# Kernel tuning notes

Measured on AMD Instinct MI355X. Metric: run time of the kernel, lower is better.

The kernel has to match this reference:

```python
import jax, jax.numpy as jnp
import numpy as np

B, D, H, W = 64, 256, 32, 32
K, DC = 1024, 128  # codebook size, codebook dim = D // 2
BETA = 0.25


def setup_inputs() -> dict:
    key = jax.random.key(0)
    ks = jax.random.split(key, 4)
    return {
        "x": jax.random.normal(ks[0], (B, D, H, W), dtype=jnp.float32),
        "pre_W": jax.random.normal(ks[1], (DC, D), dtype=jnp.float32) * (1.0 / np.sqrt(D)),
        "pre_b": jnp.zeros((DC,), dtype=jnp.float32),
        "post_W": jax.random.normal(ks[2], (D, DC), dtype=jnp.float32) * (1.0 / np.sqrt(DC)),
        "post_b": jnp.zeros((D,), dtype=jnp.float32),
        "lookup_table": jax.random.normal(ks[3], (K, DC), dtype=jnp.float32) * (1.0 / np.sqrt(DC)),
    }


def reference(x, pre_W, pre_b, post_W, post_b, lookup_table):
    sg = jax.lax.stop_gradient
    b, d, h, w = x.shape
    # pre-quant 1x1 conv: [b, d, h, w] -> [b, dc, h, w]
    z = jnp.einsum("bchw,oc->bohw", x, pre_W) + pre_b[None, :, None, None]
    # flatten tokens: [b*h*w, dc]
    zf = z.transpose(0, 2, 3, 1).reshape(-1, DC)
    # squared distances to codebook (argmin identical to cdist argmin)
    d2 = (
        jnp.sum(zf * zf, axis=1, keepdims=True)
        - 2.0 * zf @ lookup_table.T
        + jnp.sum(lookup_table * lookup_table, axis=1)[None, :]
    )  # [N, K]
    q = jnp.argmin(d2, axis=1)  # [N]
    x_e = lookup_table[q].reshape(b, h, w, DC).transpose(0, 3, 1, 2)  # [b, dc, h, w]
    # losses (enable_ema_update = False path)
    codebook_loss = jnp.mean((sg(z) - x_e) ** 2)
    commitment_loss = BETA * jnp.mean((z - sg(x_e)) ** 2)
    loss = (1.0 - BETA) * codebook_loss + commitment_loss
    # straight-through estimator
    z_st = z + sg(x_e - z)
    # post-quant 1x1 conv: [b, dc, h, w] -> [b, d, h, w]
    out = jnp.einsum("bchw,oc->bohw", z_st, post_W) + post_b[None, :, None, None]
    # perplexity from empirical code usage
    counts = jnp.zeros((K,), dtype=jnp.float32).at[q].add(1.0)
    e_mean = counts / q.shape[0]
    perplexity = jnp.exp(-jnp.sum(e_mean * jnp.log(e_mean + 1e-10)))
    q_map = q.reshape(b, h, w)
    return out, loss, q_map, perplexity
```

## Files before the change

### kernel.cpp

```cpp
#include <hip/hip_runtime.h>
#include <cstdint>

#define NB   64
#define ND   256
#define NHW  1024
#define NTOK 65536
#define NDC  128
#define NK   1024

#define OFF_LOSS 16777216
#define OFF_Q    16777217
#define OFF_PERP 16842753

#define GAPTHR 1e-3f
#define NEGINF (-3.402823466e38f)

typedef short short8 __attribute__((ext_vector_type(8)));
typedef float f32x4 __attribute__((ext_vector_type(4)));

__device__ __forceinline__ unsigned short f2bf(float f) {
  unsigned u = __float_as_uint(f);
  u += 0x7FFFu + ((u >> 16) & 1u);
  return (unsigned short)(u >> 16);
}
__device__ __forceinline__ float bf2f(unsigned short h) {
  return __uint_as_float(((unsigned)h) << 16);
}

__device__ __forceinline__ void gll16(const void* g, void* l) {
  __builtin_amdgcn_global_load_lds(
      (const __attribute__((address_space(1))) unsigned int*)g,
      (__attribute__((address_space(3))) unsigned int*)l, 16, 0, 0);
}

__global__ __launch_bounds__(256) void k_init(
    const float* __restrict__ lut, const float* __restrict__ preW,
    const float* __restrict__ postW,
    unsigned short* __restrict__ ch,
    unsigned short* __restrict__ pwh, unsigned short* __restrict__ pwl,
    unsigned short* __restrict__ qwh, unsigned short* __restrict__ qwl,
    float* __restrict__ nhn, double* __restrict__ cn2d,
    int* __restrict__ counts, double* __restrict__ lossAcc, int* __restrict__ ctr) {
  int tid = blockIdx.x * 256 + threadIdx.x;
  int stride = gridDim.x * 256;
  for (int i = tid; i < NK * NDC; i += stride) {
    int code = i >> 7, c = i & 127;
    float f = lut[i];
    unsigned short h1 = f2bf(f);
    float r = f - bf2f(h1);
    ch[code * 256 + c] = h1;
    ch[code * 256 + 128 + c] = f2bf(r);
  }
  for (int i = tid; i < NDC * ND; i += stride) {
    float f = preW[i];
    unsigned u = __float_as_uint(f);
    float lf = f - __uint_as_float(u & 0xffff0000u);
    pwh[i] = (unsigned short)(u >> 16);
    pwl[i] = (unsigned short)(__float_as_uint(lf) >> 16);
  }
  for (int i = tid; i < ND * NDC; i += stride) {
    float f = postW[i];
    unsigned u = __float_as_uint(f);
    float lf = f - __uint_as_float(u & 0xffff0000u);
    qwh[i] = (unsigned short)(u >> 16);
    qwl[i] = (unsigned short)(__float_as_uint(lf) >> 16);
  }
  if (tid < NK) {
    float s = 0.f;
    double sd = 0.0;
    for (int c = 0; c < NDC; c++) {
      float v = lut[tid * NDC + c];
      s = fmaf(v, v, s);
      sd = fma((double)v, (double)v, sd);
    }
    nhn[tid] = -0.5f * s;
    cn2d[tid] = sd;
    counts[tid] = 0;
  }
  if (tid == 0) { *lossAcc = 0.0; *ctr = 0; }
}

__global__ __launch_bounds__(256, 2) void k_preconv(
    const float* __restrict__ x, const unsigned short* __restrict__ pwh,
    const unsigned short* __restrict__ pwl, const float* __restrict__ pre_b,
    float* __restrict__ zf) {
  int bx = blockIdx.x;
  int b = bx >> 3, p0 = (bx & 7) * 128;
  int tid = threadIdx.x;
  int lane = tid & 63, w = tid >> 6;
  int g = lane >> 4, l15 = lane & 15;
  const float* xb = x + (size_t)b * (ND * NHW);
  f32x4 acc[8][2];
  #pragma unroll
  for (int rt = 0; rt < 8; ++rt)
    #pragma unroll
    for (int ct = 0; ct < 2; ++ct) acc[rt][ct] = (f32x4){0.f, 0.f, 0.f, 0.f};

  for (int ks = 0; ks < 8; ++ks) {
    int k0 = ks * 32;
    short8 bh[2], bl[2];
    #pragma unroll
    for (int ct = 0; ct < 2; ++ct) {
      int p = p0 + w * 32 + ct * 16 + l15;
      float xv[8];
      #pragma unroll
      for (int j = 0; j < 8; ++j)
        xv[j] = xb[(k0 + g * 8 + j) * NHW + p];
      #pragma unroll
      for (int j = 0; j < 8; ++j) {
        unsigned u = __float_as_uint(xv[j]);
        float lf = xv[j] - __uint_as_float(u & 0xffff0000u);
        bh[ct][j] = (short)(u >> 16);
        bl[ct][j] = (short)(__float_as_uint(lf) >> 16);
      }
    }
    #pragma unroll
    for (int rt = 0; rt < 8; ++rt) {
      short8 ah = *reinterpret_cast<const short8*>(&pwh[(rt * 16 + l15) * ND + k0 + g * 8]);
      short8 al = *reinterpret_cast<const short8*>(&pwl[(rt * 16 + l15) * ND + k0 + g * 8]);
      #pragma unroll
      for (int ct = 0; ct < 2; ++ct) {
        acc[rt][ct] = __builtin_amdgcn_mfma_f32_16x16x32_bf16(ah, bh[ct], acc[rt][ct], 0, 0, 0);
        acc[rt][ct] = __builtin_amdgcn_mfma_f32_16x16x32_bf16(ah, bl[ct], acc[rt][ct], 0, 0, 0);
        acc[rt][ct] = __builtin_amdgcn_mfma_f32_16x16x32_bf16(al, bh[ct], acc[rt][ct], 0, 0, 0);
      }
    }
  }
  #pragma unroll
  for (int rt = 0; rt < 8; ++rt) {
    float4 bb = *reinterpret_cast<const float4*>(&pre_b[rt * 16 + g * 4]);
    #pragma unroll
    for (int ct = 0; ct < 2; ++ct) {
      int n = bx * 128 + w * 32 + ct * 16 + l15;
      float4 v;
      v.x = acc[rt][ct][0] + bb.x;
      v.y = acc[rt][ct][1] + bb.y;
      v.z = acc[rt][ct][2] + bb.z;
      v.w = acc[rt][ct][3] + bb.w;
      *reinterpret_cast<float4*>(&zf[(size_t)n * NDC + rt * 16 + g * 4]) = v;
    }
  }
}

__global__ __launch_bounds__(256, 2) void k_dist(
    const float* __restrict__ zf, const unsigned short* __restrict__ ch,
    const float* __restrict__ nhn,
    int* __restrict__ q, int* __restrict__ list, int* __restrict__ ctr) {
  __shared__ __align__(16) short chbuf[2][16384];
  __shared__ float HnLds[NK];
  int tid = threadIdx.x;
  int lane = tid & 63, w = tid >> 6;
  int g = lane >> 4;
  int n0 = blockIdx.x * 128;

  for (int i = tid; i < NK; i += 256) HnLds[i] = nhn[i];

  short8 az[2][8];
  {
    int arow = lane & 15;
    #pragma unroll
    for (int rt = 0; rt < 2; ++rt) {
      const float* zr = zf + (size_t)(n0 + w * 32 + rt * 16 + arow) * NDC;
      #pragma unroll
      for (int f = 0; f < 4; ++f) {
        const float* p = zr + f * 32 + g * 8;
        float4 v0 = *reinterpret_cast<const float4*>(p);
        float4 v1 = *reinterpret_cast<const float4*>(p + 4);
        float vv[8] = {v0.x, v0.y, v0.z, v0.w, v1.x, v1.y, v1.z, v1.w};
        short8 hi, lo;
        #pragma unroll
        for (int j = 0; j < 8; ++j) {
          unsigned short h1 = f2bf(vv[j]);
          float r = vv[j] - bf2f(h1);
          hi[j] = (short)h1;
          lo[j] = (short)f2bf(r);
        }
        az[rt][f] = hi;
        az[rt][4 + f] = lo;
      }
    }
  }

  float best[2][4], sec[2][4];
  int bidx[2][4];
  #pragma unroll
  for (int rt = 0; rt < 2; ++rt)
    #pragma unroll
    for (int r = 0; r < 4; ++r) { best[rt][r] = NEGINF; sec[rt][r] = NEGINF; bidx[rt][r] = 0; }

  const char* chg = (const char*)ch;
  {
    const char* gb = chg + 0;
    #pragma unroll
    for (int rr = 0; rr < 8; ++rr) {
      int o = rr * 4096 + tid * 16;
      int so = o ^ (((o >> 9) & 7) << 4);
      gll16(gb + so, ((char*)&chbuf[0][0]) + o);
    }
  }
  asm volatile("s_waitcnt vmcnt(0)" ::: "memory");
  __syncthreads();

  int cur = 0;
  for (int chunk = 0; chunk < 16; ++chunk) {
    if (chunk < 15) {
      const char* gb = chg + (chunk + 1) * 32768;
      #pragma unroll
      for (int rr = 0; rr < 8; ++rr) {
        int o = rr * 4096 + tid * 16;
        int so = o ^ (((o >> 9) & 7) << 4);
        gll16(gb + so, ((char*)&chbuf[cur ^ 1][0]) + o);
      }
    }
    const char* cb = (const char*)&chbuf[cur][0];
    for (int ct = 0; ct < 4; ++ct) {
      int codeg = chunk * 64 + ct * 16 + (lane & 15);
      float nh = HnLds[codeg];
      short8 bc[8];
      #pragma unroll
      for (int f = 0; f < 8; ++f) {
        int byte = ((lane & 15) + ct * 16) * 512 + f * 64 + g * 16;
        byte ^= ((lane & 7) << 4);
        bc[f] = *reinterpret_cast<const short8*>(cb + byte);
      }
      f32x4 acc0 = {nh, nh, nh, nh};
      f32x4 acc1 = {nh, nh, nh, nh};
      #pragma unroll
      for (int j = 0; j < 4; ++j) {
        acc0 = __builtin_amdgcn_mfma_f32_16x16x32_bf16(az[0][j], bc[j], acc0, 0, 0, 0);
        acc1 = __builtin_amdgcn_mfma_f32_16x16x32_bf16(az[1][j], bc[j], acc1, 0, 0, 0);
        acc0 = __builtin_amdgcn_mfma_f32_16x16x32_bf16(az[0][j], bc[4 + j], acc0, 0, 0, 0);
        acc1 = __builtin_amdgcn_mfma_f32_16x16x32_bf16(az[1][j], bc[4 + j], acc1, 0, 0, 0);
        acc0 = __builtin_amdgcn_mfma_f32_16x16x32_bf16(az[0][4 + j], bc[j], acc0, 0, 0, 0);
        acc1 = __builtin_amdgcn_mfma_f32_16x16x32_bf16(az[1][4 + j], bc[j], acc1, 0, 0, 0);
      }
      #pragma unroll
      for (int r = 0; r < 4; ++r) {
        float s0 = acc0[r];
        bool t0 = s0 > best[0][r];
        bidx[0][r] = t0 ? codeg : bidx[0][r];
        sec[0][r] = fmaxf(sec[0][r], fminf(s0, best[0][r]));
        best[0][r] = fmaxf(s0, best[0][r]);
        float s1 = acc1[r];
        bool t1 = s1 > best[1][r];
        bidx[1][r] = t1 ? codeg : bidx[1][r];
        sec[1][r] = fmaxf(sec[1][r], fminf(s1, best[1][r]));
        best[1][r] = fmaxf(s1, best[1][r]);
      }
    }
    asm volatile("s_waitcnt vmcnt(0)" ::: "memory");
    __syncthreads();
    cur ^= 1;
  }

  #pragma unroll
  for (int rt = 0; rt < 2; ++rt) {
    #pragma unroll
    for (int r = 0; r < 4; ++r) {
      float b = best[rt][r];
      float s2 = sec[rt][r];
      int bi_ = bidx[rt][r];
      #pragma unroll
      for (int m = 1; m < 16; m <<= 1) {
        float ob = __shfl_xor(b, m, 64);
        float os = __shfl_xor(s2, m, 64);
        int oi = __shfl_xor(bi_, m, 64);
        float ns = fmaxf(fmaxf(s2, os), fminf(b, ob));
        bool take = (ob > b) || (ob == b && oi < bi_);
        b = take ? ob : b;
        bi_ = take ? oi : bi_;
        s2 = ns;
      }
      if ((lane & 15) == 0) {
        int token = n0 + w * 32 + rt * 16 + g * 4 + r;
        q[token] = bi_;
        if (b - s2 < GAPTHR) {
          int pos = atomicAdd(ctr, 1);
          list[pos] = token;
        }
      }
    }
  }
}

__global__ __launch_bounds__(256) void k_rescore(
    const float* __restrict__ x, const float* __restrict__ preW,
    const float* __restrict__ pre_b, const float* __restrict__ lut,
    const double* __restrict__ cn2d,
    const int* __restrict__ list, const int* __restrict__ ctr, int* __restrict__ q) {
  __shared__ float xs[4][256];
  __shared__ double zs[4][128];
  __shared__ double rd[4][256];
  __shared__ int    rc[4][256];
  int nf = *ctr;
  int tid = threadIdx.x;
  int w = tid >> 6, lane = tid & 63;
  for (int g0 = blockIdx.x * 4; g0 < nf; g0 += gridDim.x * 4) {
    int nt = nf - g0; if (nt > 4) nt = 4;
    #pragma unroll
    for (int t = 0; t < 4; ++t) {
      int token = list[g0 + (t < nt ? t : 0)];
      int b = token >> 10, p = token & 1023;
      xs[t][tid] = x[(size_t)(b * ND + tid) * NHW + p];
    }
    __syncthreads();
    #pragma unroll
    for (int rep = 0; rep < 2; ++rep) {
      int idx = rep * 256 + tid;
      int t = idx >> 7, dc = idx & 127;
      double acc = (double)pre_b[dc];
      const float* wr = preW + (size_t)dc * ND;
      #pragma unroll 4
      for (int d = 0; d < ND; d += 4) {
        float4 wv = *reinterpret_cast<const float4*>(wr + d);
        acc = fma((double)wv.x, (double)xs[t][d + 0], acc);
        acc = fma((double)wv.y, (double)xs[t][d + 1], acc);
        acc = fma((double)wv.z, (double)xs[t][d + 2], acc);
        acc = fma((double)wv.w, (double)xs[t][d + 3], acc);
      }
      zs[t][dc] = acc;
    }
    __syncthreads();
    double bd[4]; int bc_[4];
    #pragma unroll
    for (int t = 0; t < 4; ++t) { bd[t] = 1e300; bc_[t] = 0x7fffffff; }
    for (int cc = 0; cc < 4; ++cc) {
      int c = cc * 256 + tid;
      const float* cr = lut + (size_t)c * NDC;
      double a0 = 0.0, a1 = 0.0, a2 = 0.0, a3 = 0.0;
      #pragma unroll 4
      for (int k = 0; k < NDC; ++k) {
        double lc = (double)cr[k];
        a0 = fma(zs[0][k], lc, a0);
        a1 = fma(zs[1][k], lc, a1);
        a2 = fma(zs[2][k], lc, a2);
        a3 = fma(zs[3][k], lc, a3);
      }
      double cn = cn2d[c];
      double d0 = cn - 2.0 * a0; if (d0 < bd[0]) { bd[0] = d0; bc_[0] = c; }
      double d1 = cn - 2.0 * a1; if (d1 < bd[1]) { bd[1] = d1; bc_[1] = c; }
      double d2 = cn - 2.0 * a2; if (d2 < bd[2]) { bd[2] = d2; bc_[2] = c; }
      double d3 = cn - 2.0 * a3; if (d3 < bd[3]) { bd[3] = d3; bc_[3] = c; }
    }
    #pragma unroll
    for (int t = 0; t < 4; ++t) { rd[t][tid] = bd[t]; rc[t][tid] = bc_[t]; }
    __syncthreads();
    {
      double b_ = rd[w][lane]; int c_ = rc[w][lane];
      #pragma unroll
      for (int s = 64; s < 256; s += 64) {
        double ob = rd[w][lane + s]; int oc = rc[w][lane + s];
        if (ob < b_ || (ob == b_ && oc < c_)) { b_ = ob; c_ = oc; }
      }
      #pragma unroll
      for (int m = 1; m < 64; m <<= 1) {
        double ob = __shfl_xor(b_, m, 64);
        int oc = __shfl_xor(c_, m, 64);
        if (ob < b_ || (ob == b_ && oc < c_)) { b_ = ob; c_ = oc; }
      }
      if (lane == 0 && w < nt) q[list[g0 + w]] = c_;
    }
    __syncthreads();
  }
}

__global__ __launch_bounds__(256, 2) void k_post(
    const float* __restrict__ zf, const float* __restrict__ lut,
    const int* __restrict__ q, const unsigned short* __restrict__ qwh,
    const unsigned short* __restrict__ qwl, const float* __restrict__ post_b,
    float* __restrict__ out, double* __restrict__ lossAcc,
    int* __restrict__ counts, float* __restrict__ outq) {
  __shared__ float red[256];
  int bx = blockIdx.x;
  int n0 = (bx >> 1) * 128;
  int oh = (bx & 1) * 128;
  int b = n0 >> 10, p0 = n0 & 1023;
  int tid = threadIdx.x;
  int lane = tid & 63, w = tid >> 6;
  int g = lane >> 4, l15 = lane & 15;

  int qv[2];
  #pragma unroll
  for (int ct = 0; ct < 2; ++ct) qv[ct] = q[n0 + w * 32 + ct * 16 + l15];

  f32x4 acc[8][2];
  #pragma unroll
  for (int nt = 0; nt < 8; ++nt)
    #pragma unroll
    for (int ct = 0; ct < 2; ++ct) acc[nt][ct] = (f32x4){0.f, 0.f, 0.f, 0.f};

  for (int ks = 0; ks < 4; ++ks) {
    int k0 = ks * 32;
    short8 ah[2], al[2];
    #pragma unroll
    for (int ct = 0; ct < 2; ++ct) {
      const float* xr = lut + (size_t)qv[ct] * NDC + k0 + g * 8;
      float4 v0 = *reinterpret_cast<const float4*>(xr);
      float4 v1 = *reinterpret_cast<const float4*>(xr + 4);
      float vv[8] = {v0.x, v0.y, v0.z, v0.w, v1.x, v1.y, v1.z, v1.w};
      #pragma unroll
      for (int j = 0; j < 8; ++j) {
        unsigned u = __float_as_uint(vv[j]);
        float lf = vv[j] - __uint_as_float(u & 0xffff0000u);
        ah[ct][j] = (short)(u >> 16);
        al[ct][j] = (short)(__float_as_uint(lf) >> 16);
      }
    }
    #pragma unroll
    for (int nt = 0; nt < 8; ++nt) {
      short8 bh = *reinterpret_cast<const short8*>(&qwh[(size_t)(oh + nt * 16 + l15) * NDC + k0 + g * 8]);
      short8 bl = *reinterpret_cast<const short8*>(&qwl[(size_t)(oh + nt * 16 + l15) * NDC + k0 + g * 8]);
      #pragma unroll
      for (int ct = 0; ct < 2; ++ct) {
        acc[nt][ct] = __builtin_amdgcn_mfma_f32_16x16x32_bf16(ah[ct], bh, acc[nt][ct], 0, 0, 0);
        acc[nt][ct] = __builtin_amdgcn_mfma_f32_16x16x32_bf16(al[ct], bh, acc[nt][ct], 0, 0, 0);
        acc[nt][ct] = __builtin_amdgcn_mfma_f32_16x16x32_bf16(ah[ct], bl, acc[nt][ct], 0, 0, 0);
      }
    }
  }
  #pragma unroll
  for (int nt = 0; nt < 8; ++nt) {
    int o = oh + nt * 16 + l15;
    float bias = post_b[o];
    float* orow = out + (size_t)(b * ND + o) * NHW;
    #pragma unroll
    for (int ct = 0; ct < 2; ++ct) {
      int p = p0 + w * 32 + ct * 16 + g * 4;
      float4 v;
      v.x = acc[nt][ct][0] + bias;
      v.y = acc[nt][ct][1] + bias;
      v.z = acc[nt][ct][2] + bias;
      v.w = acc[nt][ct][3] + bias;
      *reinterpret_cast<float4*>(orow + p) = v;
    }
  }
  if (oh == 0) {
    if (tid < 128) {
      int n = n0 + tid;
      int c = q[n];
      atomicAdd(&counts[c], 1);
      outq[n] = (float)c;
    }
    float lp = 0.f;
    int t = tid >> 1, hf = tid & 1;
    int n = n0 + t;
    const float* zr = zf + (size_t)n * NDC + hf * 64;
    const float* cr = lut + (size_t)q[n] * NDC + hf * 64;
    #pragma unroll
    for (int i = 0; i < 16; ++i) {
      float4 zz = *reinterpret_cast<const float4*>(zr + i * 4);
      float4 xe = *reinterpret_cast<const float4*>(cr + i * 4);
      float d0 = zz.x - xe.x, d1 = zz.y - xe.y, d2 = zz.z - xe.z, d3 = zz.w - xe.w;
      lp += d0 * d0 + d1 * d1 + d2 * d2 + d3 * d3;
    }
    red[tid] = lp;
    __syncthreads();
    for (int s = 128; s > 0; s >>= 1) {
      if (tid < s) red[tid] += red[tid + s];
      __syncthreads();
    }
    if (tid == 0) atomicAdd(lossAcc, (double)red[0]);
  }
}

__global__ __launch_bounds__(256) void k_fin(
    const double* __restrict__ lossAcc, const int* __restrict__ counts,
    float* __restrict__ out_loss, float* __restrict__ out_perp) {
  __shared__ float red[256];
  int tid = threadIdx.x;
  float h = 0.f;
  for (int i = tid; i < NK; i += 256) {
    float e = (float)counts[i] * (1.0f / (float)NTOK);
    h += e * logf(e + 1e-10f);
  }
  red[tid] = h;
  __syncthreads();
  for (int s = 128; s > 0; s >>= 1) {
    if (tid < s) red[tid] += red[tid + s];
    __syncthreads();
  }
  if (tid == 0) {
    *out_perp = expf(-red[0]);
    *out_loss = (float)(*lossAcc / ((double)NTOK * (double)NDC));
  }
}

extern "C" void kernel_launch(void* const* d_in, const int* in_sizes, int n_in,
                              void* d_out, int out_size, void* d_ws, size_t ws_size,
                              hipStream_t stream) {
  const float* x     = (const float*)d_in[0];
  const float* preW  = (const float*)d_in[1];
  const float* preb  = (const float*)d_in[2];
  const float* postW = (const float*)d_in[3];
  const float* postb = (const float*)d_in[4];
  const float* lut   = (const float*)d_in[5];
  float* out = (float*)d_out;

  char* ws = (char*)d_ws;
  float*          zf      = (float*)(ws);
  unsigned short* ch      = (unsigned short*)(ws + 33554432);
  unsigned short* pwh     = (unsigned short*)(ws + 34078720);
  unsigned short* pwl     = (unsigned short*)(ws + 34144256);
  unsigned short* qwh     = (unsigned short*)(ws + 34209792);
  unsigned short* qwl     = (unsigned short*)(ws + 34275328);
  float*          nhn     = (float*)(ws + 34340864);
  int*            q       = (int*)  (ws + 34344960);
  int*            list    = (int*)  (ws + 34607104);
  int*            counts  = (int*)  (ws + 34869248);
  double*         lossAcc = (double*)(ws + 34873344);
  int*            ctr     = (int*)  (ws + 34873352);
  double*         cn2d    = (double*)(ws + 34873360);

  float* out_loss = out + OFF_LOSS;
  float* out_q    = out + OFF_Q;
  float* out_perp = out + OFF_PERP;

  hipLaunchKernelGGL(k_init, dim3(512), dim3(256), 0, stream,
                     lut, preW, postW, ch, pwh, pwl, qwh, qwl, nhn, cn2d,
                     counts, lossAcc, ctr);
  hipLaunchKernelGGL(k_preconv, dim3(512), dim3(256), 0, stream, x, pwh, pwl, preb, zf);
  hipLaunchKernelGGL(k_dist, dim3(512), dim3(256), 0, stream, zf, ch, nhn, q, list, ctr);
  hipLaunchKernelGGL(k_rescore, dim3(1024), dim3(256), 0, stream,
                     x, preW, preb, lut, cn2d, list, ctr, q);
  hipLaunchKernelGGL(k_post, dim3(1024), dim3(256), 0, stream,
                     zf, lut, q, qwh, qwl, postb, out, lossAcc, counts, out_q);
  hipLaunchKernelGGL(k_fin, dim3(1), dim3(256), 0, stream, lossAcc, counts, out_loss, out_perp);
}
```

Before: 221.2 us.

## Fold loss into distance kernel via norm identity, retile preconv, rebalance post

The loss is now computed inside k_dist from the identity ||z-c||^2 = ||z||^2 - 2*best. The squared token norms are gathered while z is converted to bf16 and reduced per block into lossAcc. This removes k_post's second pass over zf and the codebook gather for the loss. k_preconv is retiled to 64 tokens per block with twice the grid and a higher occupancy hint. k_post's code counting is spread across both output-half blocks. The loss now uses the split-bf16 best score from before rescoring, so it can differ slightly for near-tie tokens, and the norm-based form adds float cancellation error.

```diff
diff --git a/kernel.cpp b/kernel.cpp
--- a/kernel.cpp
+++ b/kernel.cpp
@@ -80,28 +80,25 @@
   if (tid == 0) { *lossAcc = 0.0; *ctr = 0; }
 }
 
-__global__ __launch_bounds__(256, 2) void k_preconv(
+__global__ __launch_bounds__(256, 4) void k_preconv(
     const float* __restrict__ x, const unsigned short* __restrict__ pwh,
     const unsigned short* __restrict__ pwl, const float* __restrict__ pre_b,
     float* __restrict__ zf) {
   int bx = blockIdx.x;
-  int b = bx >> 3, p0 = (bx & 7) * 128;
+  int b = bx >> 4, p0 = (bx & 15) * 64;
   int tid = threadIdx.x;
   int lane = tid & 63, w = tid >> 6;
   int g = lane >> 4, l15 = lane & 15;
   const float* xb = x + (size_t)b * (ND * NHW);
-  f32x4 acc[8][2];
-  #pragma unroll
-  for (int rt = 0; rt < 8; ++rt)
-    #pragma unroll
-    for (int ct = 0; ct < 2; ++ct) acc[rt][ct] = (f32x4){0.f, 0.f, 0.f, 0.f};
-
+  f32x4 acc[8];
+  #pragma unroll
+  for (int rt = 0; rt < 8; ++rt) acc[rt] = (f32x4){0.f, 0.f, 0.f, 0.f};
+
+  int p = p0 + w * 16 + l15;
   for (int ks = 0; ks < 8; ++ks) {
     int k0 = ks * 32;
-    short8 bh[2], bl[2];
-    #pragma unroll
-    for (int ct = 0; ct < 2; ++ct) {
-      int p = p0 + w * 32 + ct * 16 + l15;
+    short8 bh, bl;
+    {
       float xv[8];
       #pragma unroll
       for (int j = 0; j < 8; ++j)
@@ -110,44 +107,41 @@
       for (int j = 0; j < 8; ++j) {
         unsigned u = __float_as_uint(xv[j]);
         float lf = xv[j] - __uint_as_float(u & 0xffff0000u);
-        bh[ct][j] = (short)(u >> 16);
-        bl[ct][j] = (short)(__float_as_uint(lf) >> 16);
+        bh[j] = (short)(u >> 16);
+        bl[j] = (short)(__float_as_uint(lf) >> 16);
       }
     }
     #pragma unroll
     for (int rt = 0; rt < 8; ++rt) {
       short8 ah = *reinterpret_cast<const short8*>(&pwh[(rt * 16 + l15) * ND + k0 + g * 8]);
       short8 al = *reinterpret_cast<const short8*>(&pwl[(rt * 16 + l15) * ND + k0 + g * 8]);
-      #pragma unroll
-      for (int ct = 0; ct < 2; ++ct) {
-        acc[rt][ct] = __builtin_amdgcn_mfma_f32_16x16x32_bf16(ah, bh[ct], acc[rt][ct], 0, 0, 0);
-        acc[rt][ct] = __builtin_amdgcn_mfma_f32_16x16x32_bf16(ah, bl[ct], acc[rt][ct], 0, 0, 0);
-        acc[rt][ct] = __builtin_amdgcn_mfma_f32_16x16x32_bf16(al, bh[ct], acc[rt][ct], 0, 0, 0);
-      }
-    }
-  }
+      acc[rt] = __builtin_amdgcn_mfma_f32_16x16x32_bf16(ah, bh, acc[rt], 0, 0, 0);
+      acc[rt] = __builtin_amdgcn_mfma_f32_16x16x32_bf16(ah, bl, acc[rt], 0, 0, 0);
+      acc[rt] = __builtin_amdgcn_mfma_f32_16x16x32_bf16(al, bh, acc[rt], 0, 0, 0);
+    }
+  }
+  int n = bx * 64 + w * 16 + l15;
   #pragma unroll
   for (int rt = 0; rt < 8; ++rt) {
     float4 bb = *reinterpret_cast<const float4*>(&pre_b[rt * 16 + g * 4]);
-    #pragma unroll
-    for (int ct = 0; ct < 2; ++ct) {
-      int n = bx * 128 + w * 32 + ct * 16 + l15;
-      float4 v;
-      v.x = acc[rt][ct][0] + bb.x;
-      v.y = acc[rt][ct][1] + bb.y;
-      v.z = acc[rt][ct][2] + bb.z;
-      v.w = acc[rt][ct][3] + bb.w;
-      *reinterpret_cast<float4*>(&zf[(size_t)n * NDC + rt * 16 + g * 4]) = v;
-    }
+    float4 v;
+    v.x = acc[rt][0] + bb.x;
+    v.y = acc[rt][1] + bb.y;
+    v.z = acc[rt][2] + bb.z;
+    v.w = acc[rt][3] + bb.w;
+    *reinterpret_cast<float4*>(&zf[(size_t)n * NDC + rt * 16 + g * 4]) = v;
   }
 }
 
 __global__ __launch_bounds__(256, 2) void k_dist(
     const float* __restrict__ zf, const unsigned short* __restrict__ ch,
     const float* __restrict__ nhn,
-    int* __restrict__ q, int* __restrict__ list, int* __restrict__ ctr) {
+    int* __restrict__ q, int* __restrict__ list, int* __restrict__ ctr,
+    double* __restrict__ lossAcc) {
   __shared__ __align__(16) short chbuf[2][16384];
   __shared__ float HnLds[NK];
+  __shared__ float zn2Lds[4][2][16];
+  __shared__ float red[256];
   int tid = threadIdx.x;
   int lane = tid & 63, w = tid >> 6;
   int g = lane >> 4;
@@ -161,6 +155,7 @@
     #pragma unroll
     for (int rt = 0; rt < 2; ++rt) {
       const float* zr = zf + (size_t)(n0 + w * 32 + rt * 16 + arow) * NDC;
+      float sq = 0.f;
       #pragma unroll
       for (int f = 0; f < 4; ++f) {
         const float* p = zr + f * 32 + g * 8;
@@ -170,6 +165,7 @@
         short8 hi, lo;
         #pragma unroll
         for (int j = 0; j < 8; ++j) {
+          sq = fmaf(vv[j], vv[j], sq);
           unsigned short h1 = f2bf(vv[j]);
           float r = vv[j] - bf2f(h1);
           hi[j] = (short)h1;
@@ -178,6 +174,9 @@
         az[rt][f] = hi;
         az[rt][4 + f] = lo;
       }
+      sq += __shfl_xor(sq, 16, 64);
+      sq += __shfl_xor(sq, 32, 64);
+      if (g == 0) zn2Lds[w][rt][arow] = sq;
     }
   }
 
@@ -253,6 +252,7 @@
     cur ^= 1;
   }
 
+  float lsum = 0.f;
   #pragma unroll
   for (int rt = 0; rt < 2; ++rt) {
     #pragma unroll
@@ -278,9 +278,17 @@
           int pos = atomicAdd(ctr, 1);
           list[pos] = token;
         }
-      }
-    }
-  }
+        lsum += zn2Lds[w][rt][g * 4 + r] - 2.0f * b;
+      }
+    }
+  }
+  red[tid] = lsum;
+  __syncthreads();
+  for (int s = 128; s > 0; s >>= 1) {
+    if (tid < s) red[tid] += red[tid + s];
+    __syncthreads();
+  }
+  if (tid == 0) atomicAdd(lossAcc, (double)red[0]);
 }
 
 __global__ __launch_bounds__(256) void k_rescore(
@@ -364,13 +372,12 @@
   }
 }
 
-__global__ __launch_bounds__(256, 2) void k_post(
-    const float* __restrict__ zf, const float* __restrict__ lut,
+__global__ __launch_bounds__(256, 4) void k_post(
+    const float* __restrict__ lut,
     const int* __restrict__ q, const unsigned short* __restrict__ qwh,
     const unsigned short* __restrict__ qwl, const float* __restrict__ post_b,
-    float* __restrict__ out, double* __restrict__ lossAcc,
+    float* __restrict__ out,
     int* __restrict__ counts, float* __restrict__ outq) {
-  __shared__ float red[256];
   int bx = blockIdx.x;
   int n0 = (bx >> 1) * 128;
   int oh = (bx & 1) * 128;
@@ -382,6 +389,13 @@
   int qv[2];
   #pragma unroll
   for (int ct = 0; ct < 2; ++ct) qv[ct] = q[n0 + w * 32 + ct * 16 + l15];
+
+  if (tid < 64) {
+    int n = n0 + ((bx & 1) << 6) + tid;
+    int c = q[n];
+    atomicAdd(&counts[c], 1);
+    outq[n] = (float)c;
+  }
 
   f32x4 acc[8][2];
   #pragma unroll
@@ -433,33 +447,6 @@
       v.w = acc[nt][ct][3] + bias;
       *reinterpret_cast<float4*>(orow + p) = v;
     }
-  }
-  if (oh == 0) {
-    if (tid < 128) {
-      int n = n0 + tid;
-      int c = q[n];
-      atomicAdd(&counts[c], 1);
-      outq[n] = (float)c;
-    }
-    float lp = 0.f;
-    int t = tid >> 1, hf = tid & 1;
-    int n = n0 + t;
-    const float* zr = zf + (size_t)n * NDC + hf * 64;
-    const float* cr = lut + (size_t)q[n] * NDC + hf * 64;
-    #pragma unroll
-    for (int i = 0; i < 16; ++i) {
-      float4 zz = *reinterpret_cast<const float4*>(zr + i * 4);
-      float4 xe = *reinterpret_cast<const float4*>(cr + i * 4);
-      float d0 = zz.x - xe.x, d1 = zz.y - xe.y, d2 = zz.z - xe.z, d3 = zz.w - xe.w;
-      lp += d0 * d0 + d1 * d1 + d2 * d2 + d3 * d3;
-    }
-    red[tid] = lp;
-    __syncthreads();
-    for (int s = 128; s > 0; s >>= 1) {
-      if (tid < s) red[tid] += red[tid + s];
-      __syncthreads();
-    }
-    if (tid == 0) atomicAdd(lossAcc, (double)red[0]);
   }
 }
 
@@ -518,11 +505,11 @@
   hipLaunchKernelGGL(k_init, dim3(512), dim3(256), 0, stream,
                      lut, preW, postW, ch, pwh, pwl, qwh, qwl, nhn, cn2d,
                      counts, lossAcc, ctr);
-  hipLaunchKernelGGL(k_preconv, dim3(512), dim3(256), 0, stream, x, pwh, pwl, preb, zf);
-  hipLaunchKernelGGL(k_dist, dim3(512), dim3(256), 0, stream, zf, ch, nhn, q, list, ctr);
+  hipLaunchKernelGGL(k_preconv, dim3(1024), dim3(256), 0, stream, x, pwh, pwl, preb, zf);
+  hipLaunchKernelGGL(k_dist, dim3(512), dim3(256), 0, stream, zf, ch, nhn, q, list, ctr, lossAcc);
   hipLaunchKernelGGL(k_rescore, dim3(1024), dim3(256), 0, stream,
                      x, preW, preb, lut, cn2d, list, ctr, q);
   hipLaunchKernelGGL(k_post, dim3(1024), dim3(256), 0, stream,
-                     zf, lut, q, qwh, qwl, postb, out, lossAcc, counts, out_q);
+                     lut, q, qwh, qwl, postb, out, counts, out_q);
   hipLaunchKernelGGL(k_fin, dim3(1), dim3(256), 0, stream, lossAcc, counts, out_loss, out_perp);
 }
```

Result: slower. 233.1 us (+5.4%).
